# Performance work log

Measured on AMD Instinct MI355X. Metric: run time of the kernel, lower is better.

The kernel has to match this reference:

```python
import jax, jax.numpy as jnp
import numpy as np

# Module hyperparameters (from init_kwargs)
IN_C = 64
OUT_C = 64
K = 3
STRIDE = 1
PAD = 1
DIL = 1
OVERLAP = 4
CENTER_SIZE = 4

# Input sizes
B, H, W = 16, 128, 128


def _crop_mask(h, w):
    """Static (trace-time) crop mask: zeros on the central crop window, ones elsewhere.

    Matches the intended semantics of CropConv's python-loop mask: rows
    [crop_start, crop_start+crop_size) x cols [crop_start, crop_start+crop_size)
    of the HxW output grid are zeroed.
    """
    crop_start = (h - h // CENTER_SIZE) // 2 - OVERLAP  # 44 for h=128
    crop_size = h // CENTER_SIZE + 2 * OVERLAP          # 40 for h=128
    m = np.ones((h, w), dtype=np.float32)
    m[crop_start:crop_start + crop_size, crop_start:crop_start + crop_size] = 0.0
    return jnp.asarray(m)


def setup_inputs() -> dict:
    key = jax.random.key(0)
    kx, kw = jax.random.split(key)
    x = jax.random.normal(kx, (B, IN_C, H, W), dtype=jnp.float32)
    # kaiming_normal_ fan_out init: std = sqrt(2 / (out_channels * k * k))
    w_std = np.sqrt(2.0 / (OUT_C * K * K)).astype(np.float32)
    weight = jax.random.normal(kw, (OUT_C, IN_C, K, K), dtype=jnp.float32) * w_std
    return {"x": x, "weight": weight}


def reference(x, weight):
    # im2col (Unfold) + matmul == a standard dense conv; use the fused conv primitive.
    out = jax.lax.conv_general_dilated(
        x, weight,
        window_strides=(STRIDE, STRIDE),
        padding=((PAD, PAD), (PAD, PAD)),
        rhs_dilation=(DIL, DIL),
        dimension_numbers=("NCHW", "OIHW", "NCHW"),
    )  # [B, OUT_C, H, W] (same-size conv)
    mask = _crop_mask(out.shape[2], out.shape[3])  # [H, W], {0,1}
    # torch.where(mask, out, 0) == out * mask (mask is constant wrt grads)
    return out * mask
```

## Files before the change

kernel.cpp:

```cpp
#include <hip/hip_runtime.h>
#include <stdint.h>


#define B_ 16
#define C_ 64
#define H_ 128
#define W_ 128

#define TROWS 6
#define TCOLS 66
#define XLDS_U4 (TROWS * TCOLS * 8)

typedef float f32x4 __attribute__((ext_vector_type(4)));
typedef short bf16x8 __attribute__((ext_vector_type(8)));

__device__ inline unsigned short f2bf(float f) {
    union { float f; uint32_t u; } v; v.f = f;
    uint32_t u = v.u + 0x7FFF + ((v.u >> 16) & 1);
    return (unsigned short)(u >> 16);
}

__global__ __launch_bounds__(256) void xform_weight(
    const float* __restrict__ wgt, uint16_t* __restrict__ Wb)
{
    int L = blockIdx.x * 256 + threadIdx.x;
    int e    = L & 7;
    int lane = (L >> 3) & 63;
    int i    = (L >> 9) & 3;
    int ch   = (L >> 11) & 1;
    int kk   = L >> 12;
    int oc   = i * 16 + (lane & 15);
    int ic   = ch * 32 + (lane >> 4) * 8 + e;
    Wb[L] = f2bf(wgt[((size_t)oc * 64 + ic) * 9 + kk]);
}

__global__ __launch_bounds__(256, 3) void conv_main(
    const uint4* __restrict__ Wq,
    const float* __restrict__ x,
    float* __restrict__ out)
{
    __shared__ uint4 lds[XLDS_U4];

    const int t    = threadIdx.x;
    const int lane = t & 63;
    const int wv   = t >> 6;
    const int n    = lane & 15;
    const int q    = lane >> 4;

    const int d    = blockIdx.x;
    const int orig = (d & 7) * 128 + (d >> 3);
    const int wsd  = orig & 1;
    const int ht   = (orig >> 1) & 31;
    const int b    = orig >> 6;
    const int h0   = ht * 4;

    {
        const int cc_   = (t & 63) + 1;
        const int jh    = (t >> 6) & 1;
        const int rtri  = (t >> 7) * 3;
        const int wglob = wsd * 64 + (t & 63);
        #pragma unroll
        for (int rr = 0; rr < 3; ++rr) {
            const int r = rtri + rr;
            const int h = h0 - 1 + r;
            if (h < 0 || h >= H_) {
                uint4 z; z.x = z.y = z.z = z.w = 0;
                #pragma unroll
                for (int jj = 0; jj < 4; ++jj)
                    lds[(r * TCOLS + cc_) * 8 + ((jh * 4 + jj + cc_) & 7)] = z;
            } else {
                const float* src = x + (((size_t)b * C_) * H_ + h) * W_ + wglob;
                #pragma unroll
                for (int jj = 0; jj < 4; ++jj) {
                    const int j = jh * 4 + jj;
                    uint32_t u[4];
                    #pragma unroll
                    for (int p = 0; p < 4; ++p) {
                        float v0 = src[(size_t)(j * 8 + 2 * p)     * (H_ * W_)];
                        float v1 = src[(size_t)(j * 8 + 2 * p + 1) * (H_ * W_)];
                        u[p] = (uint32_t)f2bf(v0) | ((uint32_t)f2bf(v1) << 16);
                    }
                    lds[(r * TCOLS + cc_) * 8 + ((j + cc_) & 7)] = *(const uint4*)u;
                }
            }
        }
        if (t < 96) {
            const int j  = t & 7;
            const int r  = (t >> 3) % 6;
            const int ce = (t >= 48) ? (TCOLS - 1) : 0;
            const int h  = h0 - 1 + r;
            const int wg = wsd * 64 + ce - 1;
            uint4 val; val.x = val.y = val.z = val.w = 0;
            if (h >= 0 && h < H_ && wg >= 0 && wg < W_) {
                const float* src = x + (((size_t)b * C_) * H_ + h) * W_ + wg;
                uint32_t u[4];
                #pragma unroll
                for (int p = 0; p < 4; ++p) {
                    float v0 = src[(size_t)(j * 8 + 2 * p)     * (H_ * W_)];
                    float v1 = src[(size_t)(j * 8 + 2 * p + 1) * (H_ * W_)];
                    u[p] = (uint32_t)f2bf(v0) | ((uint32_t)f2bf(v1) << 16);
                }
                val = *(const uint4*)u;
            }
            lds[(r * TCOLS + ce) * 8 + ((j + ce) & 7)] = val;
        }
    }
    __syncthreads();

    f32x4 acc[4][4];
    #pragma unroll
    for (int i = 0; i < 4; ++i)
        #pragma unroll
        for (int f = 0; f < 4; ++f)
            acc[i][f] = (f32x4){0.f, 0.f, 0.f, 0.f};

    const int wbh   = (wv & 1) * 32;
    const int hbase = (wv >> 1) * 2;

    #pragma unroll
    for (int kh = 0; kh < 3; ++kh) {
        #pragma unroll
        for (int kw = 0; kw < 3; ++kw) {
            const int kk = kh * 3 + kw;
            #pragma unroll
            for (int ch = 0; ch < 2; ++ch) {
                bf16x8 a[4], bb[4];
                #pragma unroll
                for (int i = 0; i < 4; ++i)
                    a[i] = __builtin_bit_cast(bf16x8,
                        Wq[((kk * 2 + ch) * 4 + i) * 64 + lane]);
                #pragma unroll
                for (int f = 0; f < 4; ++f) {
                    const int hh  = f >> 1, tt = f & 1;
                    const int row = hbase + hh + kh;
                    const int ct  = wbh + tt * 16 + n + kw;
                    const int idx = (row * TCOLS + ct) * 8 + ((ch * 4 + q + ct) & 7);
                    bb[f] = __builtin_bit_cast(bf16x8, lds[idx]);
                }
                #pragma unroll
                for (int i = 0; i < 4; ++i)
                    #pragma unroll
                    for (int f = 0; f < 4; ++f)
                        acc[i][f] = __builtin_amdgcn_mfma_f32_16x16x32_bf16(
                            a[i], bb[f], acc[i][f], 0, 0, 0);
            }
        }
    }

    #pragma unroll
    for (int f = 0; f < 4; ++f) {
        const int hh = f >> 1, tt = f & 1;
        const int h  = h0 + hbase + hh;
        const int w0 = wsd * 64 + wbh + tt * 16 + n;
        const bool zz = (h >= 44 && h < 84) && (w0 >= 44 && w0 < 84);
        #pragma unroll
        for (int i = 0; i < 4; ++i) {
            #pragma unroll
            for (int r = 0; r < 4; ++r) {
                const int oc = i * 16 + q * 4 + r;
                out[(((size_t)b * C_ + oc) * H_ + h) * W_ + w0] =
                    zz ? 0.f : acc[i][f][r];
            }
        }
    }
}

#define WLDS_U4 4608
#define FXLDS_U4 4096

__global__ __launch_bounds__(256, 1) void conv_fused(
    const float* __restrict__ x,
    const float* __restrict__ wgt,
    float* __restrict__ out)
{
    __shared__ uint4 lds[WLDS_U4 + FXLDS_U4];
    uint16_t* lds16 = (uint16_t*)lds;

    const int t    = threadIdx.x;
    const int lane = t & 63;
    const int wv   = t >> 6;
    const int n    = lane & 15;
    const int q    = lane >> 4;

    const int d    = blockIdx.x;
    const int orig = (d & 7) * 128 + (d >> 3);
    const int b    = orig >> 6;
    const int h0   = (orig & 63) * 2;

    #pragma unroll
    for (int p = 0; p < 2; ++p) {
        const int a_  = t + 256 * p;
        const int oc  = a_ >> 3;
        const int oct = a_ & 7;
        const float* src = wgt + (size_t)oc * 576 + (size_t)oct * 72;
        f32x4 w4[18];
        #pragma unroll
        for (int j = 0; j < 18; ++j) w4[j] = ((const f32x4*)src)[j];
        const int ch = oct >> 2, qq = oct & 3;
        const int ii = oc >> 4,  nn = oc & 15;
        #pragma unroll
        for (int kk = 0; kk < 9; ++kk) {
            #define WELEM(e) ((uint32_t)f2bf(w4[((e)*9 + kk) >> 2][((e)*9 + kk) & 3]))
            uint4 val;
            val.x = WELEM(0) | (WELEM(1) << 16);
            val.y = WELEM(2) | (WELEM(3) << 16);
            val.z = WELEM(4) | (WELEM(5) << 16);
            val.w = WELEM(6) | (WELEM(7) << 16);
            #undef WELEM
            lds[((kk * 2 + ch) * 4 + ii) * 64 + qq * 16 + nn] = val;
        }
    }

    {
        const int ic    = t >> 2;
        const int w0    = (t & 3) * 32;
        const int jslot = ic >> 3;
        const int esub  = ic & 7;
        #pragma unroll
        for (int r = 0; r < 4; ++r) {
            const int h = h0 - 1 + r;
            if (h < 0 || h >= H_) {
                uint4 z; z.x = z.y = z.z = z.w = 0;
                #pragma unroll
                for (int k = 0; k < 4; ++k)
                    lds[WLDS_U4 + r * 1024 + k * 256 + t] = z;
            } else {
                const float* src =
                    x + (((size_t)(b * C_ + ic)) * H_ + h) * W_ + w0;
                f32x4 v4[8];
                #pragma unroll
                for (int j = 0; j < 8; ++j) v4[j] = ((const f32x4*)src)[j];
                #pragma unroll
                for (int k = 0; k < 32; ++k) {
                    const int c    = w0 + k;
                    const int slot = (jslot + c) & 7;
                    lds16[WLDS_U4 * 8 + ((r * 128 + c) * 8 + slot) * 8 + esub] =
                        f2bf(v4[k >> 2][k & 3]);
                }
            }
        }
    }
    __syncthreads();

    f32x4 acc[4][4];
    #pragma unroll
    for (int i = 0; i < 4; ++i)
        #pragma unroll
        for (int tt = 0; tt < 4; ++tt)
            acc[i][tt] = (f32x4){0.f, 0.f, 0.f, 0.f};

    const int wb = (wv & 1) * 64;
    const uint4* Wl = lds;
    const uint4* Xl = lds + WLDS_U4;
    const bool lz = (wb + n) == 0;
    const bool rz = (wb + n) == 79;
    const bf16x8 zfrag = 0;

    #pragma unroll
    for (int kh = 0; kh < 3; ++kh) {
        const int row = (wv >> 1) + kh;
        #pragma unroll
        for (int kw = 0; kw < 3; ++kw) {
            const int kk = kh * 3 + kw;
            #pragma unroll
            for (int ch = 0; ch < 2; ++ch) {
                bf16x8 a[4], bb[4];
                #pragma unroll
                for (int i = 0; i < 4; ++i)
                    a[i] = __builtin_bit_cast(bf16x8,
                        Wl[((kk * 2 + ch) * 4 + i) * 64 + lane]);
                #pragma unroll
                for (int tt = 0; tt < 4; ++tt) {
                    int c   = wb + tt * 16 + n + kw - 1;
                    int cc  = min(max(c, 0), 127);
                    int idx = (row * 128 + cc) * 8 + ((ch * 4 + q + cc) & 7);
                    bf16x8 v = __builtin_bit_cast(bf16x8, Xl[idx]);
                    if (kw == 0 && tt == 0) v = lz ? zfrag : v;
                    if (kw == 2 && tt == 3) v = rz ? zfrag : v;
                    bb[tt] = v;
                }
                #pragma unroll
                for (int i = 0; i < 4; ++i)
                    #pragma unroll
                    for (int tt = 0; tt < 4; ++tt)
                        acc[i][tt] = __builtin_amdgcn_mfma_f32_16x16x32_bf16(
                            a[i], bb[tt], acc[i][tt], 0, 0, 0);
            }
        }
    }

    const int  h  = h0 + (wv >> 1);
    const bool hz = (h >= 44 && h < 84);
    #pragma unroll
    for (int i = 0; i < 4; ++i) {
        #pragma unroll
        for (int tt = 0; tt < 4; ++tt) {
            const int  w0 = wb + tt * 16 + n;
            const bool zz = hz && (w0 >= 44 && w0 < 84);
            #pragma unroll
            for (int r = 0; r < 4; ++r) {
                const int oc = i * 16 + q * 4 + r;
                out[(((size_t)b * C_ + oc) * H_ + h) * W_ + w0] =
                    zz ? 0.f : acc[i][tt][r];
            }
        }
    }
}

extern "C" void kernel_launch(void* const* d_in, const int* in_sizes, int n_in,
                              void* d_out, int out_size, void* d_ws, size_t ws_size,
                              hipStream_t stream) {
    const float* x   = (const float*)d_in[0];
    const float* wgt = (const float*)d_in[1];
    float* out       = (float*)d_out;

    const size_t W_BYTES = 9 * 2 * 4 * 64 * 16;
    if (ws_size >= W_BYTES) {
        uint16_t* Wb = (uint16_t*)d_ws;
        xform_weight<<<dim3(144), dim3(256), 0, stream>>>(wgt, Wb);
        conv_main<<<dim3(1024), dim3(256), 0, stream>>>(
            (const uint4*)Wb, x, out);
    } else {
        conv_fused<<<dim3(1024), dim3(256), 0, stream>>>(x, wgt, out);
    }
}
```

Baseline: 130.6 us.

## Shrink conv tile to 32 columns, split output channels across waves, vectorize staging

Each block now covers 4 rows by 32 columns instead of 64 columns, and the grid doubles to 2048 blocks. Each wave computes half of the output channels (two 16-row MFMA groups) over the full 32-wide tile, which halves the accumulator registers. Launch bounds now request 6 blocks per SM, up from 3. Input staging uses float4 vector loads of four consecutive columns per channel instead of scalar loads. The cost is more halo traffic per output, because the halo columns are now a larger share of each tile, and each wave gets less MFMA reuse out of each B fragment.

Result: slower. 210.1 us (+60.9%).

```diff
diff --git a/kernel.cpp b/kernel.cpp
--- a/kernel.cpp
+++ b/kernel.cpp
@@ -8,7 +8,7 @@
 #define W_ 128
 
 #define TROWS 6
-#define TCOLS 66
+#define TCOLS 34
 #define XLDS_U4 (TROWS * TCOLS * 8)
 
 typedef float f32x4 __attribute__((ext_vector_type(4)));
@@ -34,7 +34,7 @@
     Wb[L] = f2bf(wgt[((size_t)oc * 64 + ic) * 9 + kk]);
 }
 
-__global__ __launch_bounds__(256, 3) void conv_main(
+__global__ __launch_bounds__(256, 6) void conv_main(
     const uint4* __restrict__ Wq,
     const float* __restrict__ x,
     float* __restrict__ out)
@@ -48,73 +48,83 @@
     const int q    = lane >> 4;
 
     const int d    = blockIdx.x;
-    const int orig = (d & 7) * 128 + (d >> 3);
-    const int wsd  = orig & 1;
-    const int ht   = (orig >> 1) & 31;
-    const int b    = orig >> 6;
+    const int orig = (d & 7) * 256 + (d >> 3);
+    const int wt   = orig & 3;
+    const int ht   = (orig >> 2) & 31;
+    const int b    = orig >> 7;
     const int h0   = ht * 4;
 
     {
-        const int cc_   = (t & 63) + 1;
-        const int jh    = (t >> 6) & 1;
-        const int rtri  = (t >> 7) * 3;
-        const int wglob = wsd * 64 + (t & 63);
-        #pragma unroll
-        for (int rr = 0; rr < 3; ++rr) {
-            const int r = rtri + rr;
+        const int c4    = t & 7;
+        const int j     = (t >> 3) & 7;
+        const int rr    = t >> 6;
+        const int cbase = 1 + c4 * 4;
+        const int wg0   = wt * 32 + c4 * 4;
+
+        #pragma unroll
+        for (int pass = 0; pass < 2; ++pass) {
+            const int r = rr + pass * 4;
+            if (pass == 1 && rr >= 2) break;
             const int h = h0 - 1 + r;
             if (h < 0 || h >= H_) {
                 uint4 z; z.x = z.y = z.z = z.w = 0;
                 #pragma unroll
-                for (int jj = 0; jj < 4; ++jj)
-                    lds[(r * TCOLS + cc_) * 8 + ((jh * 4 + jj + cc_) & 7)] = z;
+                for (int cc = 0; cc < 4; ++cc)
+                    lds[(r * TCOLS + cbase + cc) * 8 + ((j + cbase + cc) & 7)] = z;
             } else {
-                const float* src = x + (((size_t)b * C_) * H_ + h) * W_ + wglob;
-                #pragma unroll
-                for (int jj = 0; jj < 4; ++jj) {
-                    const int j = jh * 4 + jj;
+                const float* src =
+                    x + (((size_t)(b * C_ + j * 8)) * H_ + h) * W_ + wg0;
+                f32x4 f[8];
+                #pragma unroll
+                for (int e = 0; e < 8; ++e)
+                    f[e] = *(const f32x4*)(src + (size_t)e * (H_ * W_));
+                #pragma unroll
+                for (int cc = 0; cc < 4; ++cc) {
                     uint32_t u[4];
                     #pragma unroll
-                    for (int p = 0; p < 4; ++p) {
-                        float v0 = src[(size_t)(j * 8 + 2 * p)     * (H_ * W_)];
-                        float v1 = src[(size_t)(j * 8 + 2 * p + 1) * (H_ * W_)];
-                        u[p] = (uint32_t)f2bf(v0) | ((uint32_t)f2bf(v1) << 16);
-                    }
-                    lds[(r * TCOLS + cc_) * 8 + ((j + cc_) & 7)] = *(const uint4*)u;
-                }
-            }
-        }
-        if (t < 96) {
-            const int j  = t & 7;
-            const int r  = (t >> 3) % 6;
-            const int ce = (t >= 48) ? (TCOLS - 1) : 0;
-            const int h  = h0 - 1 + r;
-            const int wg = wsd * 64 + ce - 1;
+                    for (int p = 0; p < 4; ++p)
+                        u[p] = (uint32_t)f2bf(f[2 * p][cc]) |
+                               ((uint32_t)f2bf(f[2 * p + 1][cc]) << 16);
+                    lds[(r * TCOLS + cbase + cc) * 8 + ((j + cbase + cc) & 7)] =
+                        *(const uint4*)u;
+                }
+            }
+        }
+
+        if (t >= 128 && t < 224) {
+            const int u   = t - 128;
+            const int ce  = (u >= 48) ? (TCOLS - 1) : 0;
+            const int rem = u - (u >= 48 ? 48 : 0);
+            const int r   = rem >> 3;
+            const int jj  = rem & 7;
+            const int h   = h0 - 1 + r;
+            const int wg  = wt * 32 + ce - 1;
             uint4 val; val.x = val.y = val.z = val.w = 0;
             if (h >= 0 && h < H_ && wg >= 0 && wg < W_) {
-                const float* src = x + (((size_t)b * C_) * H_ + h) * W_ + wg;
-                uint32_t u[4];
+                const float* src =
+                    x + (((size_t)(b * C_ + jj * 8)) * H_ + h) * W_ + wg;
+                uint32_t uu[4];
                 #pragma unroll
                 for (int p = 0; p < 4; ++p) {
-                    float v0 = src[(size_t)(j * 8 + 2 * p)     * (H_ * W_)];
-                    float v1 = src[(size_t)(j * 8 + 2 * p + 1) * (H_ * W_)];
-                    u[p] = (uint32_t)f2bf(v0) | ((uint32_t)f2bf(v1) << 16);
-                }
-                val = *(const uint4*)u;
-            }
-            lds[(r * TCOLS + ce) * 8 + ((j + ce) & 7)] = val;
+                    float v0 = src[(size_t)(2 * p)     * (H_ * W_)];
+                    float v1 = src[(size_t)(2 * p + 1) * (H_ * W_)];
+                    uu[p] = (uint32_t)f2bf(v0) | ((uint32_t)f2bf(v1) << 16);
+                }
+                val = *(const uint4*)uu;
+            }
+            lds[(r * TCOLS + ce) * 8 + ((jj + ce) & 7)] = val;
         }
     }
     __syncthreads();
 
-    f32x4 acc[4][4];
-    #pragma unroll
-    for (int i = 0; i < 4; ++i)
+    f32x4 acc[2][4];
+    #pragma unroll
+    for (int i = 0; i < 2; ++i)
         #pragma unroll
         for (int f = 0; f < 4; ++f)
             acc[i][f] = (f32x4){0.f, 0.f, 0.f, 0.f};
 
-    const int wbh   = (wv & 1) * 32;
+    const int ohalf = wv & 1;
     const int hbase = (wv >> 1) * 2;
 
     #pragma unroll
@@ -124,21 +134,21 @@
             const int kk = kh * 3 + kw;
             #pragma unroll
             for (int ch = 0; ch < 2; ++ch) {
-                bf16x8 a[4], bb[4];
-                #pragma unroll
-                for (int i = 0; i < 4; ++i)
+                bf16x8 a[2], bb[4];
+                #pragma unroll
+                for (int i = 0; i < 2; ++i)
                     a[i] = __builtin_bit_cast(bf16x8,
-                        Wq[((kk * 2 + ch) * 4 + i) * 64 + lane]);
+                        Wq[((kk * 2 + ch) * 4 + ohalf * 2 + i) * 64 + lane]);
                 #pragma unroll
                 for (int f = 0; f < 4; ++f) {
                     const int hh  = f >> 1, tt = f & 1;
                     const int row = hbase + hh + kh;
-                    const int ct  = wbh + tt * 16 + n + kw;
+                    const int ct  = tt * 16 + n + kw;
                     const int idx = (row * TCOLS + ct) * 8 + ((ch * 4 + q + ct) & 7);
                     bb[f] = __builtin_bit_cast(bf16x8, lds[idx]);
                 }
                 #pragma unroll
-                for (int i = 0; i < 4; ++i)
+                for (int i = 0; i < 2; ++i)
                     #pragma unroll
                     for (int f = 0; f < 4; ++f)
                         acc[i][f] = __builtin_amdgcn_mfma_f32_16x16x32_bf16(
@@ -151,13 +161,13 @@
     for (int f = 0; f < 4; ++f) {
         const int hh = f >> 1, tt = f & 1;
         const int h  = h0 + hbase + hh;
-        const int w0 = wsd * 64 + wbh + tt * 16 + n;
+        const int w0 = wt * 32 + tt * 16 + n;
         const bool zz = (h >= 44 && h < 84) && (w0 >= 44 && w0 < 84);
         #pragma unroll
-        for (int i = 0; i < 4; ++i) {
+        for (int i = 0; i < 2; ++i) {
             #pragma unroll
             for (int r = 0; r < 4; ++r) {
-                const int oc = i * 16 + q * 4 + r;
+                const int oc = ohalf * 32 + i * 16 + q * 4 + r;
                 out[(((size_t)b * C_ + oc) * H_ + h) * W_ + w0] =
                     zz ? 0.f : acc[i][f][r];
             }
@@ -318,7 +328,7 @@
     if (ws_size >= W_BYTES) {
         uint16_t* Wb = (uint16_t*)d_ws;
         xform_weight<<<dim3(144), dim3(256), 0, stream>>>(wgt, Wb);
-        conv_main<<<dim3(1024), dim3(256), 0, stream>>>(
+        conv_main<<<dim3(2048), dim3(256), 0, stream>>>(
             (const uint4*)Wb, x, out);
     } else {
         conv_fused<<<dim3(1024), dim3(256), 0, stream>>>(x, wgt, out);
```
